# Optimization experiments

Hardware: AMD Instinct MI355X
Metric: run time of the kernel (lower is better)

Reference implementation:

```python
import jax, jax.numpy as jnp
import numpy as np

N = 50000
F = 256
E = 800000


def setup_inputs() -> dict:
    key = jax.random.key(0)
    k1, k2, k3, k4 = jax.random.split(key, 4)
    H = jax.random.normal(k1, (N, F), dtype=jnp.float32)
    H0 = jax.random.normal(k2, (N, F), dtype=jnp.float32)
    # edge list for sparse adjacency: row 0 = i (row index), row 1 = j (col index)
    edge_index = jax.random.randint(k3, (2, E), 0, N, dtype=jnp.int32)
    # W ~ U(-stdv, stdv), stdv = 1/sqrt(out_features), as in reset_parameters
    stdv = 1.0 / np.sqrt(F)
    W = jax.random.uniform(k4, (F, F), minval=-stdv, maxval=stdv, dtype=jnp.float32)
    lamda = jnp.float32(0.5)
    alpha = jnp.float32(0.1)
    l = 4
    return {"H": H, "edge_index": edge_index, "H0": H0, "W": W,
            "lamda": lamda, "alpha": alpha, "l": l}


def reference(H, edge_index, H0, W, lamda, alpha, l):
    n = H.shape[0]
    src = edge_index[0]  # i: row index of A[i, j]
    dst = edge_index[1]  # j: col index
    # A_hat = A + I ; degree = column sums of A_hat (tf.reduce_sum(A_hat, 0))
    deg = jax.ops.segment_sum(jnp.ones(src.shape[0], dtype=H.dtype), dst,
                              num_segments=n) + 1.0
    d_inv_sqrt = jax.lax.rsqrt(deg)
    # (P H)_i = d_i^{-1/2} * sum_j A[i,j] d_j^{-1/2} H_j  +  H_i / d_i  (self loop)
    msg = H[dst] * d_inv_sqrt[dst][:, None]            # [E, F]
    agg = jax.ops.segment_sum(msg, src, num_segments=n)  # [N, F]
    PH = d_inv_sqrt[:, None] * agg + H / deg[:, None]
    init_res = (1.0 - alpha) * PH + alpha * H0
    beta = jnp.log(lamda / l + 1.0)
    # init_res @ ((1-beta) I + beta W)
    output = (1.0 - beta) * init_res + beta * (init_res @ W)
    return output
```

## Files before the change

kernel.cpp:

```cpp
#include <hip/hip_runtime.h>
#include <math.h>


#define F_DIM 256
#define CHUNK 20000

typedef __attribute__((ext_vector_type(4))) float f32x4;
typedef __attribute__((ext_vector_type(8))) short short8;
typedef __attribute__((ext_vector_type(4))) unsigned short u16x4;

static __device__ __forceinline__ unsigned short f2bf(float f) {
    unsigned int u = __float_as_uint(f);
    u += 0x7fffu + ((u >> 16) & 1u);
    return (unsigned short)(u >> 16);
}
static __device__ __forceinline__ float bf2f(unsigned short u) {
    return __uint_as_float((unsigned int)u << 16);
}


__global__ __launch_bounds__(1024) void hist_kernel(
        const int* __restrict__ src, const int* __restrict__ dst,
        unsigned* __restrict__ histS, unsigned* __restrict__ histD,
        unsigned char* __restrict__ lrank, int E, int wpc4) {
    __shared__ unsigned hist[12544];
    int b = blockIdx.x;
    int which = b & 1, c = b >> 1;
    int tid = threadIdx.x;
    int e0 = c * CHUNK;
    int e1 = e0 + CHUNK < E ? e0 + CHUNK : E;
    const int* eptr = which ? dst : src;
    unsigned* outh = which ? histD : histS;

    for (int w = tid; w < wpc4; w += 1024) hist[w] = 0;
    __syncthreads();
    for (int e = e0 + tid; e < e1; e += 1024) {
        int s = eptr[e];
        int sh = (s & 3) * 8;
        unsigned old = atomicAdd(&hist[s >> 2], 1u << sh);
        if (!which) lrank[e] = (unsigned char)((old >> sh) & 0xffu);
    }
    __syncthreads();
    for (int w = tid; w < wpc4; w += 1024)
        outh[(size_t)c * wpc4 + w] = hist[w];
}


__global__ __launch_bounds__(256) void sumbase_kernel(
        const unsigned* __restrict__ histS, const unsigned* __restrict__ histD,
        int* __restrict__ cnt, float* __restrict__ dinv,
        unsigned* __restrict__ baseL, int* __restrict__ blksum,
        int wpc4, int nchunk, int n) {
    int tid = threadIdx.x;
    int w = blockIdx.x * 256 + tid;
    unsigned s0 = 0, s1 = 0, s2 = 0, s3 = 0;
    unsigned d0 = 0, d1 = 0, d2 = 0, d3 = 0;
    if (w < wpc4) {
        for (int c = 0; c < nchunk; ++c) {
            unsigned vs = histS[(size_t)c * wpc4 + w];
            unsigned vd = histD[(size_t)c * wpc4 + w];
            baseL[(size_t)c * wpc4 + w] = s0 | (s1 << 8) | (s2 << 16) | (s3 << 24);
            s0 += vs & 0xffu; s1 += (vs >> 8) & 0xffu;
            s2 += (vs >> 16) & 0xffu; s3 += vs >> 24;
            d0 += vd & 0xffu; d1 += (vd >> 8) & 0xffu;
            d2 += (vd >> 16) & 0xffu; d3 += vd >> 24;
        }
        int i0 = 4 * w;
        unsigned sv[4] = {s0, s1, s2, s3};
        unsigned dv[4] = {d0, d1, d2, d3};
        for (int k = 0; k < 4; ++k) {
            if (i0 + k < n) {
                cnt[i0 + k] = (int)sv[k];
                dinv[i0 + k] = rsqrtf((float)dv[k] + 1.0f);
            }
        }
    }
    int contrib = (w < wpc4) ? (int)(s0 + s1 + s2 + s3) : 0;
    int lane = tid & 63, wid = tid >> 6;
    int v = contrib;
    for (int off = 32; off > 0; off >>= 1) v += __shfl_down(v, off, 64);
    if (lane == 0) blksum[4 * blockIdx.x + wid] = v;
}


__global__ __launch_bounds__(256) void rowptr_kernel(const int* __restrict__ cnt,
                                                     const int* __restrict__ blksum,
                                                     int* __restrict__ row_ptr,
                                                     int n, int nb) {
    int tid = threadIdx.x;
    int lane = tid & 63, w = tid >> 6;
    int bv = (tid < nb) ? blksum[tid] : 0;
    int bs = bv;
    for (int off = 1; off < 64; off <<= 1) {
        int t = __shfl_up(bv, off, 64);
        if (lane >= off) bv += t;
    }
    __shared__ int wsb[4];
    __shared__ int sbo[256];
    if (lane == 63) wsb[w] = bv;
    __syncthreads();
    if (tid == 0) {
        int run = 0;
        for (int k = 0; k < 4; ++k) { int t = wsb[k]; wsb[k] = run; run += t; }
    }
    __syncthreads();
    sbo[tid] = wsb[w] + bv - bs;
    __syncthreads();
    int blockoff = sbo[blockIdx.x];
    int i = blockIdx.x * 256 + tid;
    int s = (i < n) ? cnt[i] : 0;
    int v = s;
    for (int off = 1; off < 64; off <<= 1) {
        int t = __shfl_up(v, off, 64);
        if (lane >= off) v += t;
    }
    __shared__ int ws[4];
    if (lane == 63) ws[w] = v;
    __syncthreads();
    if (tid == 0) {
        int run = 0;
        for (int k = 0; k < 4; ++k) { int t = ws[k]; ws[k] = run; run += t; }
    }
    __syncthreads();
    if (i <= n) row_ptr[i] = blockoff + ws[w] + v - s;
}


__global__ __launch_bounds__(256) void fillhswt_kernel(
        const int* __restrict__ src, const int* __restrict__ dst,
        const int* __restrict__ row_ptr, const unsigned char* __restrict__ baseL8,
        const unsigned char* __restrict__ lrank, int* __restrict__ col,
        const float* __restrict__ H, const float* __restrict__ dinv,
        unsigned short* __restrict__ Hs,
        const float* __restrict__ W, unsigned short* __restrict__ Wt,
        const float* __restrict__ lamda_p, const int* __restrict__ l_p,
        int E, int wpc4, int nfill, int total4) {
    int bid = blockIdx.x;
    int tid = threadIdx.x;
    if (bid < nfill) {
        int e = bid * 256 + tid;
        if (e < E) {
            int c = e / CHUNK;
            int s = src[e];
            unsigned lb = baseL8[(size_t)c * (4 * wpc4) + s];
            unsigned pos = (unsigned)row_ptr[s] + lb + lrank[e];
            col[pos] = dst[e];
        }
    } else {
        int i = (bid - nfill) * 256 + tid;
        if (i < total4) {
            int row = i >> 6;
            float d = dinv[row];
            f32x4 x = ((const f32x4*)H)[i];
            u16x4 o;
            o[0] = f2bf(x[0] * d); o[1] = f2bf(x[1] * d);
            o[2] = f2bf(x[2] * d); o[3] = f2bf(x[3] * d);
            ((u16x4*)Hs)[i] = o;
        } else {
            int t = i - total4;
            if (t < F_DIM * F_DIM) {
                float beta = logf(lamda_p[0] / (float)l_p[0] + 1.0f);
                int nn = t >> 8, kk = t & 255;
                float v = beta * W[kk * F_DIM + nn];
                if (kk == nn) v += 1.0f - beta;
                Wt[nn * F_DIM + kk] = f2bf(v);
            }
        }
    }
}


#define ACC(A, h) { A[0] += bf2f(h[0]); A[1] += bf2f(h[1]); \
                    A[2] += bf2f(h[2]); A[3] += bf2f(h[3]); }

__global__ __launch_bounds__(256) void gather_kernel(
        const unsigned short* __restrict__ Hs, const float* __restrict__ H0,
        const int* __restrict__ row_ptr, const int* __restrict__ col,
        const float* __restrict__ dinv, const float* __restrict__ alpha_p,
        unsigned short* __restrict__ irb, int n) {
    int wave = threadIdx.x >> 6;
    int lane = threadIdx.x & 63;
    int row = blockIdx.x * 4 + wave;
    if (row >= n) return;
    float alpha = alpha_p[0];
    const u16x4* Hs4 = (const u16x4*)Hs;

    int beg = row_ptr[row], end = row_ptr[row + 1];
    f32x4 a0 = 0.0f, a1 = 0.0f, a2 = 0.0f, a3 = 0.0f;
    int e = beg;
    for (; e + 8 <= end; e += 8) {
        int j0 = col[e+0], j1 = col[e+1], j2 = col[e+2], j3 = col[e+3];
        int j4 = col[e+4], j5 = col[e+5], j6 = col[e+6], j7 = col[e+7];
        u16x4 h0 = Hs4[j0*64+lane], h1 = Hs4[j1*64+lane];
        u16x4 h2 = Hs4[j2*64+lane], h3 = Hs4[j3*64+lane];
        u16x4 h4 = Hs4[j4*64+lane], h5 = Hs4[j5*64+lane];
        u16x4 h6 = Hs4[j6*64+lane], h7 = Hs4[j7*64+lane];
        ACC(a0, h0) ACC(a1, h1) ACC(a2, h2) ACC(a3, h3)
        ACC(a0, h4) ACC(a1, h5) ACC(a2, h6) ACC(a3, h7)
    }
    for (; e + 4 <= end; e += 4) {
        int j0 = col[e+0], j1 = col[e+1], j2 = col[e+2], j3 = col[e+3];
        u16x4 h0 = Hs4[j0*64+lane], h1 = Hs4[j1*64+lane];
        u16x4 h2 = Hs4[j2*64+lane], h3 = Hs4[j3*64+lane];
        ACC(a0, h0) ACC(a1, h1) ACC(a2, h2) ACC(a3, h3)
    }
    for (; e < end; ++e) {
        int j = col[e];
        u16x4 h = Hs4[j*64+lane];
        ACC(a0, h)
    }
    u16x4 hr = Hs4[row*64+lane];
    ACC(a2, hr)
    f32x4 acc = (a0 + a1) + (a2 + a3);
    float di = dinv[row];
    f32x4 h0v = __builtin_nontemporal_load((const f32x4*)H0 + row * 64 + lane);
    f32x4 init = (1.0f - alpha) * (di * acc) + alpha * h0v;
    u16x4 o;
    o[0] = f2bf(init[0]); o[1] = f2bf(init[1]);
    o[2] = f2bf(init[2]); o[3] = f2bf(init[3]);
    ((u16x4*)irb)[row * 64 + lane] = o;
}


__global__ __launch_bounds__(256) void gemm_kernel(
        const unsigned short* __restrict__ irb, const unsigned short* __restrict__ Wt,
        float* __restrict__ out, int M) {
    int w = threadIdx.x >> 6;
    int mr = blockIdx.x * 64;
    int nc = w * 64;
    int lane = threadIdx.x & 63;
    int lo = lane & 15, hi = lane >> 4;

    f32x4 acc[4][4] = {};
    for (int kk = 0; kk < 8; ++kk) {
        int kb = kk * 32 + hi * 8;
        short8 a[4], b[4];
        for (int am = 0; am < 4; ++am) {
            int row = mr + am * 16 + lo;
            a[am] = (row < M) ? *(const short8*)(irb + (size_t)row * F_DIM + kb)
                              : (short8)0;
        }
        for (int bn = 0; bn < 4; ++bn) {
            int cb = nc + bn * 16 + lo;
            b[bn] = *(const short8*)(Wt + cb * F_DIM + kb);
        }
        for (int am = 0; am < 4; ++am)
            for (int bn = 0; bn < 4; ++bn)
                acc[am][bn] = __builtin_amdgcn_mfma_f32_16x16x32_bf16(
                    a[am], b[bn], acc[am][bn], 0, 0, 0);
    }

    for (int am = 0; am < 4; ++am) {
        int rbase = mr + am * 16 + hi * 4;
        for (int r = 0; r < 4; ++r) {
            int row = rbase + r;
            if (row >= M) continue;
            for (int bn = 0; bn < 4; ++bn) {
                int c2 = nc + bn * 16 + lo;
                out[(size_t)row * F_DIM + c2] = acc[am][bn][r];
            }
        }
    }
}


extern "C" void kernel_launch(void* const* d_in, const int* in_sizes, int n_in,
                              void* d_out, int out_size, void* d_ws, size_t ws_size,
                              hipStream_t stream) {
    const float* H     = (const float*)d_in[0];
    const int*   ei    = (const int*)d_in[1];
    const float* H0    = (const float*)d_in[2];
    const float* W     = (const float*)d_in[3];
    const float* lamda = (const float*)d_in[4];
    const float* alpha = (const float*)d_in[5];
    const int*   lp    = (const int*)d_in[6];

    int n = in_sizes[0] / F_DIM;
    int E = in_sizes[1] / 2;
    const int* src = ei;
    const int* dst = ei + E;
    float* out = (float*)d_out;

    int wpc4 = (n + 3) / 4;
    int nchunk = (E + CHUNK - 1) / CHUNK;
    int nb = (n + 256) / 256;

    char* ws = (char*)d_ws;
    size_t off = 0;
    auto alloc = [&](size_t bytes) -> void* {
        void* p = ws + off;
        off += (bytes + 255) & ~(size_t)255;
        return p;
    };
    unsigned* histS = (unsigned*)alloc((size_t)nchunk * wpc4 * 4);
    unsigned* histD = (unsigned*)alloc((size_t)nchunk * wpc4 * 4);
    unsigned* baseL = (unsigned*)alloc((size_t)nchunk * wpc4 * 4);
    unsigned char* lrank = (unsigned char*)alloc((size_t)E);
    int* cnt     = (int*)alloc((size_t)n * 4);
    int* row_ptr = (int*)alloc(((size_t)n + 1) * 4);
    int* blksum  = (int*)alloc((size_t)(nb + 8) * 4);
    float* dinv  = (float*)alloc((size_t)n * 4);
    int* colb    = (int*)alloc((size_t)E * 4);
    unsigned short* Wt  = (unsigned short*)alloc((size_t)F_DIM * F_DIM * 2);
    unsigned short* Hs  = (unsigned short*)alloc((size_t)n * F_DIM * 2);
    unsigned short* irb = (unsigned short*)alloc(((size_t)n + 64) * F_DIM * 2);

    hist_kernel<<<nchunk * 2, 1024, 0, stream>>>(src, dst, histS, histD, lrank,
                                                 E, wpc4);
    int wgrid = (wpc4 + 255) / 256;
    sumbase_kernel<<<wgrid, 256, 0, stream>>>(histS, histD, cnt, dinv, baseL,
                                              blksum, wpc4, nchunk, n);
    rowptr_kernel<<<nb, 256, 0, stream>>>(cnt, blksum, row_ptr, n, nb);
    int nfill = (E + 255) / 256;
    int total4 = n * 64;
    int nhswt = (total4 + F_DIM * F_DIM + 255) / 256;
    fillhswt_kernel<<<nfill + nhswt, 256, 0, stream>>>(
        src, dst, row_ptr, (const unsigned char*)baseL, lrank, colb,
        H, dinv, Hs, W, Wt, lamda, lp, E, wpc4, nfill, total4);
    gather_kernel<<<(n + 3) / 4, 256, 0, stream>>>(Hs, H0, row_ptr, colb, dinv,
                                                   alpha, irb, n);
    int mtiles = (n + 63) / 64;
    gemm_kernel<<<mtiles, 256, 0, stream>>>(irb, Wt, out, n);
}
```

Measured before the change: 162.9 us.

## Store GEMM operands in MFMA fragment-packed layout for coalesced loads

The gather kernel now writes the init_res bf16 matrix directly into a tiled layout that matches the 16x16x32 MFMA A-fragment per lane. The W transform similarly writes Wt in B-fragment order. The GEMM then loads each fragment as one fully contiguous 16-byte-per-lane read instead of strided row reads. The cost is that the gather's stores become scattered 8-byte writes, and the tail tile reads uninitialized padding rows, which are discarded.

```diff
diff --git a/kernel.cpp b/kernel.cpp
--- a/kernel.cpp
+++ b/kernel.cpp
@@ -132,7 +132,7 @@
         const unsigned char* __restrict__ lrank, int* __restrict__ col,
         const float* __restrict__ H, const float* __restrict__ dinv,
         unsigned short* __restrict__ Hs,
-        const float* __restrict__ W, unsigned short* __restrict__ Wt,
+        const float* __restrict__ W, unsigned short* __restrict__ Wtp,
         const float* __restrict__ lamda_p, const int* __restrict__ l_p,
         int E, int wpc4, int nfill, int total4) {
     int bid = blockIdx.x;
@@ -160,10 +160,14 @@
             int t = i - total4;
             if (t < F_DIM * F_DIM) {
                 float beta = logf(lamda_p[0] / (float)l_p[0] + 1.0f);
-                int nn = t >> 8, kk = t & 255;
-                float v = beta * W[kk * F_DIM + nn];
-                if (kk == nn) v += 1.0f - beta;
-                Wt[nn * F_DIM + kk] = f2bf(v);
+                int nn = t >> 8, kf = t & 255;
+                float v = beta * W[kf * F_DIM + nn];
+                if (kf == nn) v += 1.0f - beta;
+                int cb = nn >> 4, lo = nn & 15;
+                int kk = kf >> 5, ks = kf & 31;
+                int hi = ks >> 3, el = ks & 7;
+                int lane = hi * 16 + lo;
+                Wtp[(((size_t)cb * 8 + kk) * 64 + lane) * 8 + el] = f2bf(v);
             }
         }
     }
@@ -177,7 +181,7 @@
         const unsigned short* __restrict__ Hs, const float* __restrict__ H0,
         const int* __restrict__ row_ptr, const int* __restrict__ col,
         const float* __restrict__ dinv, const float* __restrict__ alpha_p,
-        unsigned short* __restrict__ irb, int n) {
+        unsigned short* __restrict__ Af, int n) {
     int wave = threadIdx.x >> 6;
     int lane = threadIdx.x & 63;
     int row = blockIdx.x * 4 + wave;
@@ -218,43 +222,48 @@
     u16x4 o;
     o[0] = f2bf(init[0]); o[1] = f2bf(init[1]);
     o[2] = f2bf(init[2]); o[3] = f2bf(init[3]);
-    ((u16x4*)irb)[row * 64 + lane] = o;
+    size_t idx = (((size_t)((row >> 4) * 8 + (lane >> 3)) * 64)
+                  + ((lane >> 1) & 3) * 16 + (row & 15)) * 8 + (lane & 1) * 4;
+    *(u16x4*)(Af + idx) = o;
 }
 
 
 __global__ __launch_bounds__(256) void gemm_kernel(
-        const unsigned short* __restrict__ irb, const unsigned short* __restrict__ Wt,
+        const unsigned short* __restrict__ Af, const unsigned short* __restrict__ Wtp,
         float* __restrict__ out, int M) {
-    int w = threadIdx.x >> 6;
+    int tid = threadIdx.x;
+    int w = tid >> 6;
+    int lane = tid & 63;
+    int lo = lane & 15, hi = lane >> 4;
     int mr = blockIdx.x * 64;
     int nc = w * 64;
-    int lane = threadIdx.x & 63;
-    int lo = lane & 15, hi = lane >> 4;
+    int fb0 = mr >> 4;
 
     f32x4 acc[4][4] = {};
     for (int kk = 0; kk < 8; ++kk) {
-        int kb = kk * 32 + hi * 8;
         short8 a[4], b[4];
-        for (int am = 0; am < 4; ++am) {
-            int row = mr + am * 16 + lo;
-            a[am] = (row < M) ? *(const short8*)(irb + (size_t)row * F_DIM + kb)
-                              : (short8)0;
-        }
-        for (int bn = 0; bn < 4; ++bn) {
-            int cb = nc + bn * 16 + lo;
-            b[bn] = *(const short8*)(Wt + cb * F_DIM + kb);
-        }
+#pragma unroll
         for (int am = 0; am < 4; ++am)
+            a[am] = *(const short8*)(Af + (((size_t)(fb0 + am) * 8 + kk) * 64 + lane) * 8);
+#pragma unroll
+        for (int bn = 0; bn < 4; ++bn)
+            b[bn] = *(const short8*)(Wtp + (((size_t)(w * 4 + bn) * 8 + kk) * 64 + lane) * 8);
+#pragma unroll
+        for (int am = 0; am < 4; ++am)
+#pragma unroll
             for (int bn = 0; bn < 4; ++bn)
                 acc[am][bn] = __builtin_amdgcn_mfma_f32_16x16x32_bf16(
                     a[am], b[bn], acc[am][bn], 0, 0, 0);
     }
 
+#pragma unroll
     for (int am = 0; am < 4; ++am) {
         int rbase = mr + am * 16 + hi * 4;
+#pragma unroll
         for (int r = 0; r < 4; ++r) {
             int row = rbase + r;
             if (row >= M) continue;
+#pragma unroll
             for (int bn = 0; bn < 4; ++bn) {
                 int c2 = nc + bn * 16 + lo;
                 out[(size_t)row * F_DIM + c2] = acc[am][bn][r];
@@ -301,9 +310,9 @@
     int* blksum  = (int*)alloc((size_t)(nb + 8) * 4);
     float* dinv  = (float*)alloc((size_t)n * 4);
     int* colb    = (int*)alloc((size_t)E * 4);
-    unsigned short* Wt  = (unsigned short*)alloc((size_t)F_DIM * F_DIM * 2);
+    unsigned short* Wtp = (unsigned short*)alloc((size_t)F_DIM * F_DIM * 2);
     unsigned short* Hs  = (unsigned short*)alloc((size_t)n * F_DIM * 2);
-    unsigned short* irb = (unsigned short*)alloc(((size_t)n + 64) * F_DIM * 2);
+    unsigned short* Af  = (unsigned short*)alloc(((size_t)n + 64) * F_DIM * 2);
 
     hist_kernel<<<nchunk * 2, 1024, 0, stream>>>(src, dst, histS, histD, lrank,
                                                  E, wpc4);
@@ -316,9 +325,9 @@
     int nhswt = (total4 + F_DIM * F_DIM + 255) / 256;
     fillhswt_kernel<<<nfill + nhswt, 256, 0, stream>>>(
         src, dst, row_ptr, (const unsigned char*)baseL, lrank, colb,
-        H, dinv, Hs, W, Wt, lamda, lp, E, wpc4, nfill, total4);
+        H, dinv, Hs, W, Wtp, lamda, lp, E, wpc4, nfill, total4);
     gather_kernel<<<(n + 3) / 4, 256, 0, stream>>>(Hs, H0, row_ptr, colb, dinv,
-                                                   alpha, irb, n);
+                                                   alpha, Af, n);
     int mtiles = (n + 63) / 64;
-    gemm_kernel<<<mtiles, 256, 0, stream>>>(irb, Wt, out, n);
-}
+    gemm_kernel<<<mtiles, 256, 0, stream>>>(Af, Wtp, out, n);
+}
```

Result: faster. 151.1 us (-7.2%).
